# Optimization experiments

Measured on AMD Instinct MI355X. Metric: run time of the kernel, lower is better.

Reference implementation:

```python
import jax, jax.numpy as jnp
import numpy as np

N_SVC, N_NODE, N_POD = 50000, 20000, 100000
F = 128          # svc/instance/node feature dims (all 128 per init_kwargs)
HID = 128        # hidden_size
OUT = 64         # out_channel
E_SVC, E_PN, E_NP = 1600000, 100000, 100000


def _graph_conv(x, src, dst, n_src, n_dst, W, b):
    """DGL GraphConv with norm='both': D_dst^{-1/2} A D_src^{-1/2} X W + b."""
    ones = jnp.ones(src.shape[0], dtype=x.dtype)
    deg_src = jnp.clip(jax.ops.segment_sum(ones, src, num_segments=n_src), 1.0)
    deg_dst = jnp.clip(jax.ops.segment_sum(ones, dst, num_segments=n_dst), 1.0)
    # normalize at source, gather, scatter-sum to dst, normalize at dst
    h = x * jax.lax.rsqrt(deg_src)[:, None]          # [n_src, F]
    msg = h[src]                                      # [E, F] gather (memory-bound)
    agg = jax.ops.segment_sum(msg, dst, num_segments=n_dst)  # [n_dst, F]
    agg = agg * jax.lax.rsqrt(deg_dst)[:, None]
    return agg @ W + b                                # [n_dst, HID]


def _leaky(h):
    return jnp.where(h > 0, h, 0.01 * h)


def setup_inputs() -> dict:
    key = jax.random.key(0)
    ks = jax.random.split(key, 16)
    d = {
        "x_svc": jax.random.normal(ks[0], (N_SVC, F), jnp.float32),
        "x_pod": jax.random.normal(ks[1], (N_POD, F), jnp.float32),
        "x_node": jax.random.normal(ks[2], (N_NODE, F), jnp.float32),
        "svc_src": jax.random.randint(ks[3], (E_SVC,), 0, N_SVC, jnp.int32),
        "svc_dst": jax.random.randint(ks[4], (E_SVC,), 0, N_SVC, jnp.int32),
        "pod_node_src": jax.random.randint(ks[5], (E_PN,), 0, N_POD, jnp.int32),
        "pod_node_dst": jax.random.randint(ks[6], (E_PN,), 0, N_NODE, jnp.int32),
        "node_pod_src": jax.random.randint(ks[7], (E_NP,), 0, N_NODE, jnp.int32),
        "node_pod_dst": jax.random.randint(ks[8], (E_NP,), 0, N_POD, jnp.int32),
        # GraphConv weights per edge type
        "W_call": jax.random.normal(ks[9], (F, HID), jnp.float32) * (1.0 / np.sqrt(F)),
        "b_call": jnp.zeros((HID,), jnp.float32),
        "W_in": jax.random.normal(ks[10], (F, HID), jnp.float32) * (1.0 / np.sqrt(F)),
        "b_in": jnp.zeros((HID,), jnp.float32),
        "W_ni": jax.random.normal(ks[11], (F, HID), jnp.float32) * (1.0 / np.sqrt(F)),
        "b_ni": jnp.zeros((HID,), jnp.float32),
        # per-node-type output Linear (hidden -> out_channel)
        "W_lin_svc": jax.random.normal(ks[12], (HID, OUT), jnp.float32) * (1.0 / np.sqrt(HID)),
        "b_lin_svc": jnp.zeros((OUT,), jnp.float32),
        "W_lin_node": jax.random.normal(ks[13], (HID, OUT), jnp.float32) * (1.0 / np.sqrt(HID)),
        "b_lin_node": jnp.zeros((OUT,), jnp.float32),
        "W_lin_pod": jax.random.normal(ks[14], (HID, OUT), jnp.float32) * (1.0 / np.sqrt(HID)),
        "b_lin_pod": jnp.zeros((OUT,), jnp.float32),
    }
    return d


def reference(x_svc, x_pod, x_node,
              svc_src, svc_dst, pod_node_src, pod_node_dst,
              node_pod_src, node_pod_dst,
              W_call, b_call, W_in, b_in, W_ni, b_ni,
              W_lin_svc, b_lin_svc, W_lin_node, b_lin_node,
              W_lin_pod, b_lin_pod):
    # HeteroGraphConv (sum aggregate; each dst type receives one edge type here)
    h_svc = _graph_conv(x_svc, svc_src, svc_dst, N_SVC, N_SVC, W_call, b_call)
    h_node = _graph_conv(x_pod, pod_node_src, pod_node_dst, N_POD, N_NODE, W_in, b_in)
    h_pod = _graph_conv(x_node, node_pod_src, node_pod_dst, N_NODE, N_POD, W_ni, b_ni)
    # per-node-type LeakyReLU + Linear
    o_svc = _leaky(h_svc) @ W_lin_svc + b_lin_svc    # [N_SVC, OUT]
    o_node = _leaky(h_node) @ W_lin_node + b_lin_node  # [N_NODE, OUT]
    o_pod = _leaky(h_pod) @ W_lin_pod + b_lin_pod    # [N_POD, OUT]
    return jnp.concatenate([o_svc, o_node, o_pod], axis=0)  # [N_SVC+N_NODE+N_POD, OUT]
```

## Files before the change

### kernel.cpp

```cpp
#include <hip/hip_runtime.h>

typedef __attribute__((ext_vector_type(8))) short short8;
typedef __attribute__((ext_vector_type(4))) float floatx4;

#define N_SVC  50000
#define N_NODE 20000
#define N_POD  100000
#define E_SVC  1600000
#define E_PN   100000
#define E_NP   100000
#define N_TOT  170000
#define E_TOT  1800000
#define NBUCK  1329
#define NBLK   256
#define PER_BLK 7032
#define P_SVC_BASE  0
#define P_NODE_BASE 50048
#define P_POD_BASE  70080
#define P_TOT       170112
#define SVC_WAVES   50048
#define AGG_WAVES   80064
#define AGG_BLOCKS  20016

__device__ __forceinline__ unsigned short f2bf(float f) {
  union { float f; unsigned u; } v; v.f = f;
  unsigned r = v.u + 0x7FFFu + ((v.u >> 16) & 1u);
  return (unsigned short)(r >> 16);
}
__device__ __forceinline__ unsigned pack_bf2(float a, float b) {
  return (unsigned)f2bf(a) | ((unsigned)f2bf(b) << 16);
}
__device__ __forceinline__ float bfl(unsigned u) { union { unsigned u; float f; } v; v.u = u << 16; return v.f; }
__device__ __forceinline__ float bfh(unsigned u) { union { unsigned u; float f; } v; v.u = u & 0xFFFF0000u; return v.f; }

__device__ __forceinline__ int dbase_of(int b) {
  if (b <= 391) return b * 6144;
  if (b <= 547) return 2402304 + (b - 391) * 1536;
  return 2641920 + (b - 547) * 512;
}
#define DST_CAP_TOT 3042304
__device__ __forceinline__ int sbase_of(int b) {
  if (b <= 391) return b * 6144;
  if (b <= 1171) return 2402304 + (b - 391) * 512;
  return 2801664 + (b - 1171) * 1536;
}
#define SRC_CAP_TOT 3044352

__device__ __forceinline__ void load_edge(int i,
    const int* __restrict__ svcS, const int* __restrict__ svcD,
    const int* __restrict__ pnS, const int* __restrict__ pnD,
    const int* __restrict__ npS, const int* __restrict__ npD,
    int& S, int& D) {
  if (i < E_SVC)             { S = svcS[i];                         D = svcD[i]; }
  else if (i < E_SVC + E_PN) { int j = i - E_SVC;        S = pnS[j] + 50000;  D = pnD[j] + 50000; }
  else                       { int j = i - E_SVC - E_PN; S = npS[j] + 150000; D = npD[j] + 70000; }
}

__global__ void init_cur(int* __restrict__ dcur, int* __restrict__ scur) {
  int b = blockIdx.x * 1024 + threadIdx.x;
  if (b < NBUCK) { dcur[b] = dbase_of(b); scur[b] = sbase_of(b); }
}

__global__ __launch_bounds__(1024) void scatter_onepass(
    const int* __restrict__ svcS, const int* __restrict__ svcD,
    const int* __restrict__ pnS, const int* __restrict__ pnD,
    const int* __restrict__ npS, const int* __restrict__ npD,
    int* __restrict__ dcur, int* __restrict__ scur,
    unsigned* __restrict__ dstbuf, unsigned char* __restrict__ srcbuf) {
  __shared__ int ldc[NBUCK], lsc[NBUCK];
  const int tid = threadIdx.x;
  for (int t = tid; t < NBUCK; t += 1024) { ldc[t] = 0; lsc[t] = 0; }
  __syncthreads();
  const int lo = blockIdx.x * PER_BLK;
  const int hi = (lo + PER_BLK < E_TOT) ? lo + PER_BLK : E_TOT;
  int Sv[7], Dv[7];
  #pragma unroll
  for (int k = 0; k < 7; ++k) {
    int e = lo + tid + k * 1024;
    if (e < hi) {
      load_edge(e, svcS, svcD, pnS, pnD, npS, npD, Sv[k], Dv[k]);
      atomicAdd(&ldc[Dv[k] >> 7], 1);
      atomicAdd(&lsc[Sv[k] >> 7], 1);
    } else Sv[k] = -1;
  }
  __syncthreads();
  for (int t = tid; t < NBUCK; t += 1024) {
    int c = ldc[t];  ldc[t] = c ? atomicAdd(&dcur[t], c) : 0;
    int c2 = lsc[t]; lsc[t] = c2 ? atomicAdd(&scur[t], c2) : 0;
  }
  __syncthreads();
  #pragma unroll
  for (int k = 0; k < 7; ++k) {
    if (Sv[k] >= 0) {
      int p = atomicAdd(&ldc[Dv[k] >> 7], 1);
      dstbuf[p] = ((unsigned)(Dv[k] & 127) << 18) | (unsigned)Sv[k];
      int q = atomicAdd(&lsc[Sv[k] >> 7], 1);
      srcbuf[q] = (unsigned char)(Sv[k] & 127);
    }
  }
}

__global__ __launch_bounds__(256) void finalize_all(
    const int* __restrict__ dcur, const int* __restrict__ scur,
    const unsigned* __restrict__ dstbuf, const unsigned char* __restrict__ srcbuf,
    int2* __restrict__ rowrange, int* __restrict__ csr, int* __restrict__ cnt_src) {
  __shared__ int lcnt[128], lcur[128];
  __shared__ int s_w0;
  const int tid = threadIdx.x;
  if (blockIdx.x < NBUCK) {
    const int b = blockIdx.x;
    const int base = dbase_of(b);
    const int cnt = dcur[b] - base;
    if (tid < 128) lcnt[tid] = 0;
    __syncthreads();
    for (int e = tid; e < cnt; e += 256) atomicAdd(&lcnt[dstbuf[base + e] >> 18], 1);
    __syncthreads();
    int excl = 0, v = 0;
    if (tid < 128) {
      v = lcnt[tid];
      int lane = tid & 63;
      int x = v;
      #pragma unroll
      for (int off = 1; off < 64; off <<= 1) {
        int y = __shfl_up(x, off, 64);
        if (lane >= off) x += y;
      }
      excl = x - v;
      if (tid == 63) s_w0 = x;
    }
    __syncthreads();
    if (tid < 128) {
      if (tid >= 64) excl += s_w0;
      lcur[tid] = excl;
      int u = b * 128 + tid;
      if (u < N_TOT) rowrange[u] = make_int2(base + excl, base + excl + v);
    }
    __syncthreads();
    for (int e = tid; e < cnt; e += 256) {
      unsigned wv = dstbuf[base + e];
      int p = atomicAdd(&lcur[wv >> 18], 1);
      csr[base + p] = (int)(wv & 0x3FFFFu);
    }
  } else {
    const int b = blockIdx.x - NBUCK;
    const int base = sbase_of(b);
    const int cnt = scur[b] - base;
    if (tid < 128) lcnt[tid] = 0;
    __syncthreads();
    for (int e = tid; e < cnt; e += 256) atomicAdd(&lcnt[srcbuf[base + e]], 1);
    __syncthreads();
    if (tid < 128) {
      int u = b * 128 + tid;
      if (u < N_TOT) cnt_src[u] = lcnt[tid];
    }
  }
}

__global__ void normalize_cast(const float* __restrict__ xs, const float* __restrict__ xp,
                               const float* __restrict__ xn, const int* __restrict__ cs,
                               unsigned* __restrict__ Xn) {
  int i = blockIdx.x * blockDim.x + threadIdx.x;
  if (i >= N_TOT * 32) return;
  int row = i >> 5, c4 = i & 31;
  const float* src;
  if (row < 50000)       src = xs + (size_t)row * 128;
  else if (row < 150000) src = xp + (size_t)(row - 50000) * 128;
  else                   src = xn + (size_t)(row - 150000) * 128;
  int cc = cs[row]; if (cc < 1) cc = 1;
  float r = rsqrtf((float)cc);
  float4 v = ((const float4*)src)[c4];
  uint2 o;
  o.x = pack_bf2(v.x * r, v.y * r);
  o.y = pack_bf2(v.z * r, v.w * r);
  *(uint2*)(Xn + (size_t)row * 64 + c4 * 2) = o;
}

#define ACC8(v) { a0 += bfl(v.x); a1 += bfh(v.x); a2 += bfl(v.y); a3 += bfh(v.y); \
                  a4 += bfl(v.z); a5 += bfh(v.z); a6 += bfl(v.w); a7 += bfh(v.w); }

__global__ __launch_bounds__(256) void aggregate_bf16(
    const unsigned* __restrict__ Xn, const int2* __restrict__ rowrange,
    const int* __restrict__ csr, unsigned* __restrict__ aggb) {
  const int lane = threadIdx.x & 63;
  const int gwave = blockIdx.x * 4 + (threadIdx.x >> 6);
  const int grp = lane >> 4, l16 = lane & 15;
  const unsigned* Xb = Xn + l16 * 4;
  if (gwave < SVC_WAVES) {
    const int gw = gwave;
    unsigned* orow = aggb + (size_t)gw * 64 + l16 * 4;
    if (gw >= 50000) {
      if (grp == 0) *(uint4*)orow = (uint4){0u, 0u, 0u, 0u};
      return;
    }
    int2 rr = rowrange[gw];
    int beg = rr.x, end = rr.y;
    int deg = end - beg;
    float a0 = 0.f, a1 = 0.f, a2 = 0.f, a3 = 0.f, a4 = 0.f, a5 = 0.f, a6 = 0.f, a7 = 0.f;
    int e = beg;
    for (; e + 16 <= end; e += 16) {
      int sA = csr[e + grp];
      int sB = csr[e + 4 + grp];
      int sC = csr[e + 8 + grp];
      int sD = csr[e + 12 + grp];
      uint4 vA = *(const uint4*)(Xb + (unsigned)sA * 64);
      uint4 vB = *(const uint4*)(Xb + (unsigned)sB * 64);
      uint4 vC = *(const uint4*)(Xb + (unsigned)sC * 64);
      uint4 vD = *(const uint4*)(Xb + (unsigned)sD * 64);
      ACC8(vA) ACC8(vB) ACC8(vC) ACC8(vD)
    }
    for (; e + 8 <= end; e += 8) {
      int sA = csr[e + grp];
      int sB = csr[e + 4 + grp];
      uint4 vA = *(const uint4*)(Xb + (unsigned)sA * 64);
      uint4 vB = *(const uint4*)(Xb + (unsigned)sB * 64);
      ACC8(vA) ACC8(vB)
    }
    for (; e + 4 <= end; e += 4) {
      int s = csr[e + grp];
      uint4 v = *(const uint4*)(Xb + (unsigned)s * 64);
      ACC8(v)
    }
    if (grp < end - e) {
      int s = csr[e + grp];
      uint4 v = *(const uint4*)(Xb + (unsigned)s * 64);
      ACC8(v)
    }
    a0 += __shfl_xor(a0, 32, 64); a1 += __shfl_xor(a1, 32, 64);
    a2 += __shfl_xor(a2, 32, 64); a3 += __shfl_xor(a3, 32, 64);
    a4 += __shfl_xor(a4, 32, 64); a5 += __shfl_xor(a5, 32, 64);
    a6 += __shfl_xor(a6, 32, 64); a7 += __shfl_xor(a7, 32, 64);
    a0 += __shfl_xor(a0, 16, 64); a1 += __shfl_xor(a1, 16, 64);
    a2 += __shfl_xor(a2, 16, 64); a3 += __shfl_xor(a3, 16, 64);
    a4 += __shfl_xor(a4, 16, 64); a5 += __shfl_xor(a5, 16, 64);
    a6 += __shfl_xor(a6, 16, 64); a7 += __shfl_xor(a7, 16, 64);
    float rd = rsqrtf((float)(deg < 1 ? 1 : deg));
    if (grp == 0) {
      uint4 o;
      o.x = pack_bf2(a0 * rd, a1 * rd);
      o.y = pack_bf2(a2 * rd, a3 * rd);
      o.z = pack_bf2(a4 * rd, a5 * rd);
      o.w = pack_bf2(a6 * rd, a7 * rd);
      *(uint4*)orow = o;
    }
  } else {
    const int row = SVC_WAVES + (gwave - SVC_WAVES) * 4 + grp;
    int u; bool valid;
    if (row < P_POD_BASE) { u = row - 48; valid = (row - P_NODE_BASE) < 20000; }
    else                  { u = row - 80; valid = (row - P_POD_BASE) < 100000; }
    unsigned* orow = aggb + (size_t)row * 64 + l16 * 4;
    if (!valid) {
      *(uint4*)orow = (uint4){0u, 0u, 0u, 0u};
      return;
    }
    int2 rr = rowrange[u];
    int beg = rr.x, end = rr.y;
    int deg = end - beg;
    float a0 = 0.f, a1 = 0.f, a2 = 0.f, a3 = 0.f, a4 = 0.f, a5 = 0.f, a6 = 0.f, a7 = 0.f;
    int e = beg;
    for (; e + 2 <= end; e += 2) {
      int s0 = csr[e];
      int s1 = csr[e + 1];
      uint4 v0 = *(const uint4*)(Xb + (unsigned)s0 * 64);
      uint4 v1 = *(const uint4*)(Xb + (unsigned)s1 * 64);
      ACC8(v0) ACC8(v1)
    }
    if (e < end) {
      int s = csr[e];
      uint4 v = *(const uint4*)(Xb + (unsigned)s * 64);
      ACC8(v)
    }
    float rd = rsqrtf((float)(deg < 1 ? 1 : deg));
    uint4 o;
    o.x = pack_bf2(a0 * rd, a1 * rd);
    o.y = pack_bf2(a2 * rd, a3 * rd);
    o.z = pack_bf2(a4 * rd, a5 * rd);
    o.w = pack_bf2(a6 * rd, a7 * rd);
    *(uint4*)orow = o;
  }
}

__global__ void wprep(const float* __restrict__ W0, const float* __restrict__ W1,
                      const float* __restrict__ W2, const float* __restrict__ L0,
                      const float* __restrict__ L1, const float* __restrict__ L2,
                      unsigned short* __restrict__ Wt, unsigned short* __restrict__ Wt2) {
  int i = blockIdx.x * 256 + threadIdx.x;
  if (i < 3 * 16384) {
    int t = i / 16384, r = i % 16384, n = r / 128, k = r % 128;
    const float* W = (t == 0) ? W0 : ((t == 1) ? W1 : W2);
    Wt[i] = f2bf(W[k * 128 + n]);
  } else if (i < 3 * 16384 + 3 * 8192) {
    int j = i - 3 * 16384;
    int t = j / 8192, r = j % 8192, n = r / 128, k = r % 128;
    const float* L = (t == 0) ? L0 : ((t == 1) ? L1 : L2);
    Wt2[j] = f2bf(L[k * 64 + n]);
  }
}

__global__ __launch_bounds__(256) void gemm_fused(
    const unsigned short* __restrict__ aggb,
    const unsigned short* __restrict__ Wt,
    const unsigned short* __restrict__ Wt2,
    const float* __restrict__ b0, const float* __restrict__ b1, const float* __restrict__ b2,
    const float* __restrict__ l0, const float* __restrict__ l1, const float* __restrict__ l2,
    float* __restrict__ out) {
  __shared__ __align__(16) unsigned short sW1[128 * 136];
  __shared__ __align__(16) unsigned short sH[4][16 * 136];
  const int bid = blockIdx.x;
  int t, bl, nb, ntile, padbase, outbase, mcnt;
  if (bid < 226)      { t = 0; bl = bid;       nb = 226; ntile = 782;  padbase = P_SVC_BASE;  outbase = 0;     mcnt = 50000; }
  else if (bid < 316) { t = 1; bl = bid - 226; nb = 90;  ntile = 313;  padbase = P_NODE_BASE; outbase = 50000; mcnt = 20000; }
  else                { t = 2; bl = bid - 316; nb = 452; ntile = 1563; padbase = P_POD_BASE;  outbase = 70000; mcnt = 100000; }
  const float* bp = (t == 0) ? b0 : ((t == 1) ? b1 : b2);
  const float* lp = (t == 0) ? l0 : ((t == 1) ? l1 : l2);

  const unsigned short* W1g = Wt + t * 16384;
  for (int uu = threadIdx.x; uu < 2048; uu += 256) {
    short8 v = *(const short8*)(W1g + uu * 8);
    *(short8*)(&sW1[(uu >> 4) * 136 + (uu & 15) * 8]) = v;
  }
  const int wv = threadIdx.x >> 6, lane = threadIdx.x & 63;
  const int quad = lane >> 4, l16 = lane & 15;

  const unsigned short* W2g = Wt2 + t * 8192;
  short8 w2f[4][4];
  #pragma unroll
  for (int n = 0; n < 4; n++)
    #pragma unroll
    for (int kt = 0; kt < 4; kt++)
      w2f[n][kt] = *(const short8*)(W2g + (n * 16 + l16) * 128 + kt * 32 + quad * 8);
  float bias1[8], bias2[4];
  #pragma unroll
  for (int n = 0; n < 8; n++) bias1[n] = bp[n * 16 + l16];
  #pragma unroll
  for (int n = 0; n < 4; n++) bias2[n] = lp[n * 16 + l16];
  __syncthreads();

  for (int tile = bl; tile < ntile; tile += nb) {
    const unsigned short* Arow = aggb + (size_t)(padbase + tile * 64 + wv * 16 + l16) * 128;
    floatx4 acc[8];
    #pragma unroll
    for (int n = 0; n < 8; n++) acc[n] = (floatx4){0.f, 0.f, 0.f, 0.f};
    #pragma unroll
    for (int kt = 0; kt < 4; kt++) {
      short8 af = *(const short8*)(Arow + kt * 32 + quad * 8);
      #pragma unroll
      for (int n = 0; n < 8; n++) {
        short8 bf = *(const short8*)(&sW1[(n * 16 + l16) * 136 + kt * 32 + quad * 8]);
        acc[n] = __builtin_amdgcn_mfma_f32_16x16x32_bf16(af, bf, acc[n], 0, 0, 0);
      }
    }
    #pragma unroll
    for (int n = 0; n < 8; n++) {
      #pragma unroll
      for (int i = 0; i < 4; i++) {
        float h = acc[n][i] + bias1[n];
        h = (h > 0.f) ? h : 0.01f * h;
        sH[wv][(quad * 4 + i) * 136 + n * 16 + l16] = f2bf(h);
      }
    }
    floatx4 acc2[4];
    #pragma unroll
    for (int n = 0; n < 4; n++) acc2[n] = (floatx4){0.f, 0.f, 0.f, 0.f};
    #pragma unroll
    for (int kt = 0; kt < 4; kt++) {
      short8 af = *(const short8*)(&sH[wv][l16 * 136 + kt * 32 + quad * 8]);
      #pragma unroll
      for (int n = 0; n < 4; n++)
        acc2[n] = __builtin_amdgcn_mfma_f32_16x16x32_bf16(af, w2f[n][kt], acc2[n], 0, 0, 0);
    }
    int r0 = tile * 64 + wv * 16 + quad * 4;
    #pragma unroll
    for (int n = 0; n < 4; n++) {
      #pragma unroll
      for (int i = 0; i < 4; i++) {
        int r = r0 + i;
        if (r < mcnt) out[(size_t)(outbase + r) * 64 + n * 16 + l16] = acc2[n][i] + bias2[n];
      }
    }
  }
}

extern "C" void kernel_launch(void* const* d_in, const int* in_sizes, int n_in,
                              void* d_out, int out_size, void* d_ws, size_t ws_size,
                              hipStream_t stream) {
  const float* x_svc  = (const float*)d_in[0];
  const float* x_pod  = (const float*)d_in[1];
  const float* x_node = (const float*)d_in[2];
  const int* svc_src  = (const int*)d_in[3];
  const int* svc_dst  = (const int*)d_in[4];
  const int* pn_src   = (const int*)d_in[5];
  const int* pn_dst   = (const int*)d_in[6];
  const int* np_src   = (const int*)d_in[7];
  const int* np_dst   = (const int*)d_in[8];
  const float* W_call = (const float*)d_in[9];
  const float* b_call = (const float*)d_in[10];
  const float* W_in   = (const float*)d_in[11];
  const float* b_in   = (const float*)d_in[12];
  const float* W_ni   = (const float*)d_in[13];
  const float* b_ni   = (const float*)d_in[14];
  const float* W_ls   = (const float*)d_in[15];
  const float* b_ls   = (const float*)d_in[16];
  const float* W_ln   = (const float*)d_in[17];
  const float* b_ln   = (const float*)d_in[18];
  const float* W_lp   = (const float*)d_in[19];
  const float* b_lp   = (const float*)d_in[20];
  float* out = (float*)d_out;

  char* ws = (char*)d_ws;
  int*  dcur     = (int*)(ws + 0);
  int*  scur     = (int*)(ws + 5504);
  int2* rowrange = (int2*)(ws + 11008);
  int*  cnt_src  = (int*)(ws + 1371008);
  int*  csr      = (int*)(ws + 2051072);
  unsigned short* Wt  = (unsigned short*)(ws + 14220288);
  unsigned short* Wt2 = (unsigned short*)(ws + 14318592);
  unsigned* Xn     = (unsigned*)(ws + 14367744);
  unsigned* dstbuf = (unsigned*)(ws + 14367744);
  unsigned char* srcbuf = (unsigned char*)(ws + 26537088);
  unsigned* aggb   = (unsigned*)(ws + 57887744);

  init_cur<<<2, 1024, 0, stream>>>(dcur, scur);
  scatter_onepass<<<NBLK, 1024, 0, stream>>>(svc_src, svc_dst, pn_src, pn_dst,
                                             np_src, np_dst, dcur, scur, dstbuf, srcbuf);
  finalize_all<<<2 * NBUCK, 256, 0, stream>>>(dcur, scur, dstbuf, srcbuf,
                                              rowrange, csr, cnt_src);
  wprep<<<288, 256, 0, stream>>>(W_call, W_in, W_ni, W_ls, W_ln, W_lp, Wt, Wt2);
  normalize_cast<<<21250, 256, 0, stream>>>(x_svc, x_pod, x_node, cnt_src, Xn);
  aggregate_bf16<<<AGG_BLOCKS, 256, 0, stream>>>(Xn, rowrange, csr, aggb);
  gemm_fused<<<768, 256, 0, stream>>>((const unsigned short*)aggb, Wt, Wt2,
                                      b_call, b_in, b_ni, b_ls, b_ln, b_lp, out);
}
```

Before: 309.5 us.

## Coarsen CSR-build buckets from 128 to 1024 nodes and drop init kernel

The two-level counting sort that builds the destination CSR and source degree counts now uses 167 buckets of 1024 nodes instead of 1329 buckets of 128. The scatter pass therefore does fewer global atomics per block and fewer shared-memory bucket slots, and finalize runs 334 blocks of 512 threads with a two-level prefix scan. Bucket cursors now start at zero, so a memset replaces the init kernel and the base offset is added per bucket. In exchange, shared-atomic contention on the coarser buckets rises, the finalize pass has far less block-level parallelism, and each block handles up to 38400 edges.

Result: slower. 324.1 us (+4.7%).

```diff
diff --git a/kernel.cpp b/kernel.cpp
--- a/kernel.cpp
+++ b/kernel.cpp
@@ -11,7 +11,7 @@
 #define E_NP   100000
 #define N_TOT  170000
 #define E_TOT  1800000
-#define NBUCK  1329
+#define NB2    167
 #define NBLK   256
 #define PER_BLK 7032
 #define P_SVC_BASE  0
@@ -33,18 +33,18 @@
 __device__ __forceinline__ float bfl(unsigned u) { union { unsigned u; float f; } v; v.u = u << 16; return v.f; }
 __device__ __forceinline__ float bfh(unsigned u) { union { unsigned u; float f; } v; v.u = u & 0xFFFF0000u; return v.f; }
 
-__device__ __forceinline__ int dbase_of(int b) {
-  if (b <= 391) return b * 6144;
-  if (b <= 547) return 2402304 + (b - 391) * 1536;
-  return 2641920 + (b - 547) * 512;
-}
-#define DST_CAP_TOT 3042304
-__device__ __forceinline__ int sbase_of(int b) {
-  if (b <= 391) return b * 6144;
-  if (b <= 1171) return 2402304 + (b - 391) * 512;
-  return 2801664 + (b - 1171) * 1536;
-}
-#define SRC_CAP_TOT 3044352
+__device__ __forceinline__ int dbase2(int b) {
+  if (b < 49) return b * 38400;
+  if (b < 69) return 1881600 + (b - 49) * 7424;
+  return 2030080 + (b - 69) * 2048;
+}
+#define DST2_TOT 2230784
+__device__ __forceinline__ int sbase2(int b) {
+  if (b < 49) return b * 38400;
+  if (b < 146) return 1881600 + (b - 49) * 2048;
+  return 2080256 + (b - 146) * 7424;
+}
+#define SRC2_TOT 2236160
 
 __device__ __forceinline__ void load_edge(int i,
     const int* __restrict__ svcS, const int* __restrict__ svcD,
@@ -56,20 +56,15 @@
   else                       { int j = i - E_SVC - E_PN; S = npS[j] + 150000; D = npD[j] + 70000; }
 }
 
-__global__ void init_cur(int* __restrict__ dcur, int* __restrict__ scur) {
-  int b = blockIdx.x * 1024 + threadIdx.x;
-  if (b < NBUCK) { dcur[b] = dbase_of(b); scur[b] = sbase_of(b); }
-}
-
 __global__ __launch_bounds__(1024) void scatter_onepass(
     const int* __restrict__ svcS, const int* __restrict__ svcD,
     const int* __restrict__ pnS, const int* __restrict__ pnD,
     const int* __restrict__ npS, const int* __restrict__ npD,
     int* __restrict__ dcur, int* __restrict__ scur,
-    unsigned* __restrict__ dstbuf, unsigned char* __restrict__ srcbuf) {
-  __shared__ int ldc[NBUCK], lsc[NBUCK];
+    unsigned* __restrict__ dstbuf, unsigned short* __restrict__ srcbuf) {
+  __shared__ int ldc[NB2], lsc[NB2];
   const int tid = threadIdx.x;
-  for (int t = tid; t < NBUCK; t += 1024) { ldc[t] = 0; lsc[t] = 0; }
+  if (tid < NB2) { ldc[tid] = 0; lsc[tid] = 0; }
   __syncthreads();
   const int lo = blockIdx.x * PER_BLK;
   const int hi = (lo + PER_BLK < E_TOT) ? lo + PER_BLK : E_TOT;
@@ -79,80 +74,82 @@
     int e = lo + tid + k * 1024;
     if (e < hi) {
       load_edge(e, svcS, svcD, pnS, pnD, npS, npD, Sv[k], Dv[k]);
-      atomicAdd(&ldc[Dv[k] >> 7], 1);
-      atomicAdd(&lsc[Sv[k] >> 7], 1);
+      atomicAdd(&ldc[Dv[k] >> 10], 1);
+      atomicAdd(&lsc[Sv[k] >> 10], 1);
     } else Sv[k] = -1;
   }
   __syncthreads();
-  for (int t = tid; t < NBUCK; t += 1024) {
-    int c = ldc[t];  ldc[t] = c ? atomicAdd(&dcur[t], c) : 0;
-    int c2 = lsc[t]; lsc[t] = c2 ? atomicAdd(&scur[t], c2) : 0;
+  if (tid < NB2) {
+    int c = ldc[tid];  ldc[tid] = c ? (dbase2(tid) + atomicAdd(&dcur[tid], c)) : 0;
+    int c2 = lsc[tid]; lsc[tid] = c2 ? (sbase2(tid) + atomicAdd(&scur[tid], c2)) : 0;
   }
   __syncthreads();
   #pragma unroll
   for (int k = 0; k < 7; ++k) {
     if (Sv[k] >= 0) {
-      int p = atomicAdd(&ldc[Dv[k] >> 7], 1);
-      dstbuf[p] = ((unsigned)(Dv[k] & 127) << 18) | (unsigned)Sv[k];
-      int q = atomicAdd(&lsc[Sv[k] >> 7], 1);
-      srcbuf[q] = (unsigned char)(Sv[k] & 127);
-    }
-  }
-}
-
-__global__ __launch_bounds__(256) void finalize_all(
+      int p = atomicAdd(&ldc[Dv[k] >> 10], 1);
+      dstbuf[p] = ((unsigned)(Dv[k] & 1023) << 18) | (unsigned)Sv[k];
+      int q = atomicAdd(&lsc[Sv[k] >> 10], 1);
+      srcbuf[q] = (unsigned short)(Sv[k] & 1023);
+    }
+  }
+}
+
+__global__ __launch_bounds__(512) void finalize_all(
     const int* __restrict__ dcur, const int* __restrict__ scur,
-    const unsigned* __restrict__ dstbuf, const unsigned char* __restrict__ srcbuf,
+    const unsigned* __restrict__ dstbuf, const unsigned short* __restrict__ srcbuf,
     int2* __restrict__ rowrange, int* __restrict__ csr, int* __restrict__ cnt_src) {
-  __shared__ int lcnt[128], lcur[128];
-  __shared__ int s_w0;
+  __shared__ int lcnt[1024], lcur[1024];
+  __shared__ int wsum[8], woff[8];
   const int tid = threadIdx.x;
-  if (blockIdx.x < NBUCK) {
+  const int w = tid >> 6, lane = tid & 63;
+  if (blockIdx.x < NB2) {
     const int b = blockIdx.x;
-    const int base = dbase_of(b);
-    const int cnt = dcur[b] - base;
-    if (tid < 128) lcnt[tid] = 0;
-    __syncthreads();
-    for (int e = tid; e < cnt; e += 256) atomicAdd(&lcnt[dstbuf[base + e] >> 18], 1);
-    __syncthreads();
-    int excl = 0, v = 0;
-    if (tid < 128) {
-      v = lcnt[tid];
-      int lane = tid & 63;
-      int x = v;
+    const int base = dbase2(b);
+    const int cnt = dcur[b];
+    lcnt[2 * tid] = 0; lcnt[2 * tid + 1] = 0;
+    __syncthreads();
+    for (int e = tid; e < cnt; e += 512) atomicAdd(&lcnt[dstbuf[base + e] >> 18], 1);
+    __syncthreads();
+    int v0 = lcnt[2 * tid], v1 = lcnt[2 * tid + 1];
+    int s = v0 + v1;
+    int x = s;
+    #pragma unroll
+    for (int off = 1; off < 64; off <<= 1) {
+      int y = __shfl_up(x, off, 64);
+      if (lane >= off) x += y;
+    }
+    if (lane == 63) wsum[w] = x;
+    __syncthreads();
+    if (tid == 0) {
+      int acc = 0;
       #pragma unroll
-      for (int off = 1; off < 64; off <<= 1) {
-        int y = __shfl_up(x, off, 64);
-        if (lane >= off) x += y;
-      }
-      excl = x - v;
-      if (tid == 63) s_w0 = x;
-    }
-    __syncthreads();
-    if (tid < 128) {
-      if (tid >= 64) excl += s_w0;
-      lcur[tid] = excl;
-      int u = b * 128 + tid;
-      if (u < N_TOT) rowrange[u] = make_int2(base + excl, base + excl + v);
-    }
-    __syncthreads();
-    for (int e = tid; e < cnt; e += 256) {
+      for (int i = 0; i < 8; i++) { woff[i] = acc; acc += wsum[i]; }
+    }
+    __syncthreads();
+    int excl = x - s + woff[w];
+    lcur[2 * tid] = excl;
+    lcur[2 * tid + 1] = excl + v0;
+    int u0 = b * 1024 + 2 * tid;
+    if (u0 < N_TOT)     rowrange[u0]     = make_int2(base + excl, base + excl + v0);
+    if (u0 + 1 < N_TOT) rowrange[u0 + 1] = make_int2(base + excl + v0, base + excl + v0 + v1);
+    __syncthreads();
+    for (int e = tid; e < cnt; e += 512) {
       unsigned wv = dstbuf[base + e];
       int p = atomicAdd(&lcur[wv >> 18], 1);
       csr[base + p] = (int)(wv & 0x3FFFFu);
     }
   } else {
-    const int b = blockIdx.x - NBUCK;
-    const int base = sbase_of(b);
-    const int cnt = scur[b] - base;
-    if (tid < 128) lcnt[tid] = 0;
-    __syncthreads();
-    for (int e = tid; e < cnt; e += 256) atomicAdd(&lcnt[srcbuf[base + e]], 1);
-    __syncthreads();
-    if (tid < 128) {
-      int u = b * 128 + tid;
-      if (u < N_TOT) cnt_src[u] = lcnt[tid];
-    }
+    const int b = blockIdx.x - NB2;
+    const int base = sbase2(b);
+    const int cnt = scur[b];
+    lcnt[2 * tid] = 0; lcnt[2 * tid + 1] = 0;
+    __syncthreads();
+    for (int e = tid; e < cnt; e += 512) atomicAdd(&lcnt[srcbuf[base + e]], 1);
+    __syncthreads();
+    int u0 = b * 1024 + 2 * tid;
+    if (u0 < N_TOT)     cnt_src[u0]     = lcnt[2 * tid];
+    if (u0 + 1 < N_TOT) cnt_src[u0 + 1] = lcnt[2 * tid + 1];
   }
 }
 
@@ -408,22 +405,22 @@
 
   char* ws = (char*)d_ws;
   int*  dcur     = (int*)(ws + 0);
-  int*  scur     = (int*)(ws + 5504);
-  int2* rowrange = (int2*)(ws + 11008);
-  int*  cnt_src  = (int*)(ws + 1371008);
-  int*  csr      = (int*)(ws + 2051072);
-  unsigned short* Wt  = (unsigned short*)(ws + 14220288);
-  unsigned short* Wt2 = (unsigned short*)(ws + 14318592);
-  unsigned* Xn     = (unsigned*)(ws + 14367744);
-  unsigned* dstbuf = (unsigned*)(ws + 14367744);
-  unsigned char* srcbuf = (unsigned char*)(ws + 26537088);
-  unsigned* aggb   = (unsigned*)(ws + 57887744);
-
-  init_cur<<<2, 1024, 0, stream>>>(dcur, scur);
+  int*  scur     = (int*)(ws + 668);
+  int2* rowrange = (int2*)(ws + 1344);
+  int*  cnt_src  = (int*)(ws + 1361344);
+  int*  csr      = (int*)(ws + 2041344);
+  unsigned short* Wt  = (unsigned short*)(ws + 10964480);
+  unsigned short* Wt2 = (unsigned short*)(ws + 11062784);
+  unsigned* Xn     = (unsigned*)(ws + 11112448);
+  unsigned* dstbuf = (unsigned*)(ws + 11112448);
+  unsigned short* srcbuf = (unsigned short*)(ws + 20040192);
+  unsigned* aggb   = (unsigned*)(ws + 54661120);
+
+  hipMemsetAsync(dcur, 0, 1336, stream);
   scatter_onepass<<<NBLK, 1024, 0, stream>>>(svc_src, svc_dst, pn_src, pn_dst,
                                              np_src, np_dst, dcur, scur, dstbuf, srcbuf);
-  finalize_all<<<2 * NBUCK, 256, 0, stream>>>(dcur, scur, dstbuf, srcbuf,
-                                              rowrange, csr, cnt_src);
+  finalize_all<<<2 * NB2, 512, 0, stream>>>(dcur, scur, dstbuf, srcbuf,
+                                            rowrange, csr, cnt_src);
   wprep<<<288, 256, 0, stream>>>(W_call, W_in, W_ni, W_ls, W_ln, W_lp, Wt, Wt2);
   normalize_cast<<<21250, 256, 0, stream>>>(x_svc, x_pod, x_node, cnt_src, Xn);
   aggregate_bf16<<<AGG_BLOCKS, 256, 0, stream>>>(Xn, rowrange, csr, aggb);
```
